# Kernel tuning notes

Measured on AMD Instinct MI355X. Metric: run time of the kernel, lower is better.

Reference implementation:

```python
import jax, jax.numpy as jnp
import numpy as np

N = 50000      # nodes
E = 1600000    # edges (avg degree 32)
F = 64         # input node features
H = 128        # GAT hidden dim (heads=1)
A = 16         # action dim
ED = 2         # edge feature dim


def setup_inputs() -> dict:
    key = jax.random.key(0)
    ks = jax.random.split(key, 20)
    def w(k, shape, fan_in):
        return jax.random.normal(k, shape, jnp.float32) * (1.0 / np.sqrt(fan_in))
    return {
        "x": jax.random.normal(ks[0], (N, F), jnp.float32),
        "edge_index": jax.random.randint(ks[1], (2, E), 0, N, dtype=jnp.int32),
        "edge_attr": jax.random.normal(ks[2], (E, ED), jnp.float32),
        # GATConv layer 1 (F -> H)
        "W1": w(ks[3], (F, H), F),
        "We1": w(ks[4], (ED, H), ED),
        "asrc1": w(ks[5], (H,), H),
        "adst1": w(ks[6], (H,), H),
        "aedge1": w(ks[7], (H,), H),
        "b1": jnp.zeros((H,), jnp.float32),
        # GATConv layer 2 (H -> H)
        "W2": w(ks[8], (H, H), H),
        "We2": w(ks[9], (ED, H), ED),
        "asrc2": w(ks[10], (H,), H),
        "adst2": w(ks[11], (H,), H),
        "aedge2": w(ks[12], (H,), H),
        "b2": jnp.zeros((H,), jnp.float32),
        # final head
        "Wfc": w(ks[13], (H, A), H),
        "bfc": jnp.zeros((A,), jnp.float32),
    }


def _gat_layer(x, src, dst, ea, W, We, a_s, a_d, a_e, b, n):
    """PyG GATConv, heads=1: gather -> attn logits -> segment softmax -> scatter-add."""
    h = x @ W                      # [n, H]
    he = ea @ We                   # [E', H]
    logits = jax.nn.leaky_relu(
        (h * a_s).sum(-1)[src] + (h * a_d).sum(-1)[dst] + (he * a_e).sum(-1),
        negative_slope=0.2,
    )                              # [E']
    m = jax.ops.segment_max(logits, dst, num_segments=n)
    p = jnp.exp(logits - m[dst])
    denom = jax.ops.segment_sum(p, dst, num_segments=n)
    alpha = p / (denom[dst] + 1e-16)
    out = jax.ops.segment_sum(h[src] * alpha[:, None], dst, num_segments=n)
    return out + b


def reference(x, edge_index, edge_attr, W1, We1, asrc1, adst1, aedge1, b1,
              W2, We2, asrc2, adst2, aedge2, b2, Wfc, bfc):
    n = x.shape[0]
    src0, dst0 = edge_index[0], edge_index[1]
    # add_self_loops=True with fill_value='mean': self-loop edge_attr is the
    # mean of incoming edge_attr per destination node (0 if no incoming edges)
    cnt = jax.ops.segment_sum(jnp.ones_like(dst0, dtype=edge_attr.dtype), dst0, num_segments=n)
    ea_mean = jax.ops.segment_sum(edge_attr, dst0, num_segments=n) / jnp.maximum(cnt, 1.0)[:, None]
    loops = jnp.arange(n, dtype=src0.dtype)
    src = jnp.concatenate([src0, loops])
    dst = jnp.concatenate([dst0, loops])
    ea = jnp.concatenate([edge_attr, ea_mean], axis=0)

    h = jax.nn.relu(_gat_layer(x, src, dst, ea, W1, We1, asrc1, adst1, aedge1, b1, n))
    h = jax.nn.relu(_gat_layer(h, src, dst, ea, W2, We2, asrc2, adst2, aedge2, b2, n))
    pooled = h.mean(axis=0)        # [H]
    return jnp.tanh(pooled @ Wfc + bfc)
```

## Files before the change

### kernel.cpp

```cpp
#include <hip/hip_runtime.h>
#include <math.h>

#define H_DIM 128
#define BWID 128
#define BMAX 512
#define CHUNK 4096

typedef int v4i __attribute__((ext_vector_type(4)));

__global__ void prep_kernel(const float* __restrict__ We1, const float* __restrict__ ae1,
                            const float* __restrict__ We2, const float* __restrict__ ae2,
                            const float* __restrict__ W1, const float* __restrict__ as1,
                            const float* __restrict__ ad1,
                            const float* __restrict__ W2, const float* __restrict__ as2,
                            const float* __restrict__ ad2,
                            float* __restrict__ c, float* __restrict__ vs1,
                            float* __restrict__ vd1, float* __restrict__ vs2,
                            float* __restrict__ vd2) {
    int t = threadIdx.x;
    if (t < 64) {
        float s = 0.f, d = 0.f;
        for (int h = 0; h < 128; ++h) {
            float w = W1[t * 128 + h];
            s += w * as1[h];
            d += w * ad1[h];
        }
        vs1[t] = s; vd1[t] = d;
    } else if (t < 192) {
        int k = t - 64;
        float s = 0.f, d = 0.f;
        for (int h = 0; h < 128; ++h) {
            float w = W2[k * 128 + h];
            s += w * as2[h];
            d += w * ad2[h];
        }
        vs2[k] = s; vd2[k] = d;
    } else {
        int l = t - 192;
        float a1x = ae1[l], a1y = ae1[l + 64];
        float a2x = ae2[l], a2y = ae2[l + 64];
        float v0 = We1[l] * a1x + We1[l + 64] * a1y;
        float v1 = We1[128 + l] * a1x + We1[192 + l] * a1y;
        float v2 = We2[l] * a2x + We2[l + 64] * a2y;
        float v3 = We2[128 + l] * a2x + We2[192 + l] * a2y;
        for (int off = 32; off; off >>= 1) {
            v0 += __shfl_xor(v0, off);
            v1 += __shfl_xor(v1, off);
            v2 += __shfl_xor(v2, off);
            v3 += __shfl_xor(v3, off);
        }
        if (l == 0) { c[0] = v0; c[1] = v1; c[2] = v2; c[3] = v3; }
    }
}

__global__ __launch_bounds__(256) void count_kernel(const int* __restrict__ ei,
                                                    int* __restrict__ gcnt, int E, int B) {
    __shared__ int hist[BMAX];
    int tid = threadIdx.x;
    for (int i = tid; i < B; i += 256) hist[i] = 0;
    __syncthreads();
    int lo = blockIdx.x * CHUNK, hi = min(lo + CHUNK, E);
    for (int e = lo + tid; e < hi; e += 256)
        atomicAdd(&hist[ei[E + e] >> 7], 1);
    __syncthreads();
    for (int i = tid; i < B; i += 256)
        if (hist[i]) atomicAdd(&gcnt[i], hist[i]);
}

__global__ void bscan_kernel(const int* __restrict__ gcnt, int* __restrict__ bstart,
                             int* __restrict__ gcur, int* __restrict__ rowptr,
                             int B, int n, int E) {
    __shared__ int s[BMAX];
    int t = threadIdx.x;
    int v0 = (t < B) ? gcnt[t] : 0;
    s[t] = v0;
    __syncthreads();
    for (int off = 1; off < BMAX; off <<= 1) {
        int v = (t >= off) ? s[t - off] : 0;
        __syncthreads();
        s[t] += v;
        __syncthreads();
    }
    if (t < B) {
        int excl = s[t] - v0;
        bstart[t] = excl;
        gcur[t] = excl;
    }
    if (t == 0) { bstart[B] = E; rowptr[n] = E; }
}

__global__ __launch_bounds__(256) void bin_kernel(const int* __restrict__ ei,
                                                  const float* __restrict__ ea,
                                                  const float* __restrict__ cvec,
                                                  int* __restrict__ gcur,
                                                  int4* __restrict__ binned, int E, int B) {
    __shared__ int cnt[BMAX];
    __shared__ int base[BMAX];
    int tid = threadIdx.x;
    for (int i = tid; i < B; i += 256) cnt[i] = 0;
    __syncthreads();
    int lo = blockIdx.x * CHUNK, hi = min(lo + CHUNK, E);
    for (int e = lo + tid; e < hi; e += 256)
        atomicAdd(&cnt[ei[E + e] >> 7], 1);
    __syncthreads();
    for (int i = tid; i < B; i += 256) {
        int c = cnt[i];
        base[i] = c ? atomicAdd(&gcur[i], c) : 0;
        cnt[i] = 0;
    }
    __syncthreads();
    float c0 = cvec[0], c1 = cvec[1], c2 = cvec[2], c3 = cvec[3];
    for (int e = lo + tid; e < hi; e += 256) {
        int s = ei[e], d = ei[E + e];
        float2 v = ((const float2*)ea)[e];
        float d1 = c0 * v.x + c1 * v.y;
        float d2 = c2 * v.x + c3 * v.y;
        int b = d >> 7;
        int loc = atomicAdd(&cnt[b], 1);
        binned[(size_t)(base[b] + loc)] = make_int4(s, d, __float_as_int(d1), __float_as_int(d2));
    }
}

__global__ __launch_bounds__(256) void build_kernel(const int* __restrict__ bstart,
                                                    const int4* __restrict__ binned,
                                                    int* __restrict__ rowptr,
                                                    int4* __restrict__ csr, int n) {
    __shared__ int cnt[BWID];
    __shared__ int sc[BWID];
    __shared__ int cur[BWID];
    int b = blockIdx.x, tid = threadIdx.x;
    int d0 = b << 7;
    int lo = bstart[b], hi = bstart[b + 1];
    if (tid < BWID) cnt[tid] = 0;
    __syncthreads();
    for (int k = lo + tid; k < hi; k += 256)
        atomicAdd(&cnt[binned[k].y & (BWID - 1)], 1);
    __syncthreads();
    if (tid < BWID) sc[tid] = cnt[tid];
    __syncthreads();
    for (int off = 1; off < BWID; off <<= 1) {
        int v = (tid < BWID && tid >= off) ? sc[tid - off] : 0;
        __syncthreads();
        if (tid < BWID) sc[tid] += v;
        __syncthreads();
    }
    if (tid < BWID) {
        int excl = sc[tid] - cnt[tid];
        cur[tid] = lo + excl;
        int d = d0 + tid;
        if (d < n) rowptr[d] = lo + excl;
    }
    __syncthreads();
    for (int k = lo + tid; k < hi; k += 256) {
        int4 e = binned[k];
        int slot = atomicAdd(&cur[e.y & (BWID - 1)], 1);
        csr[slot] = make_int4(e.x, e.z, e.w, 0);
    }
}

__global__ void hshd64_kernel(const float* __restrict__ x, const float* __restrict__ vs,
                              const float* __restrict__ vd, float* __restrict__ hs,
                              float* __restrict__ hd, int n) {
    int w = (blockIdx.x * blockDim.x + threadIdx.x) >> 6;
    int lane = threadIdx.x & 63;
    if (w >= n) return;
    float xv = x[(size_t)w * 64 + lane];
    float ss = xv * vs[lane];
    float sd = xv * vd[lane];
    for (int off = 32; off; off >>= 1) {
        ss += __shfl_xor(ss, off);
        sd += __shfl_xor(sd, off);
    }
    if (lane == 0) { hs[w] = ss; hd[w] = sd; }
}

__global__ __launch_bounds__(256) void agg64_kernel(
        const int* __restrict__ rowptr, const int4* __restrict__ csr,
        const float* __restrict__ hs, const float* __restrict__ hd,
        const float* __restrict__ feat, float* __restrict__ t_out, int n) {
    int w = (blockIdx.x * blockDim.x + threadIdx.x) >> 6;
    int lane = threadIdx.x & 63;
    if (w >= n) return;
    int beg = rowptr[w], end = rowptr[w + 1];
    int len = end - beg;
    float hdv = hd[w], hsw = hs[w];
    int g = lane >> 4;
    int c16 = lane & 15;
    float4 acc = make_float4(0.f, 0.f, 0.f, 0.f);
    float m, scale, lself;

    if (len <= 64) {
        bool valid = lane < len;
        int4 c4 = valid ? csr[beg + lane] : make_int4(0, 0, 0, 0);
        float ed = valid ? __int_as_float(c4.y) : 0.f;
        float l = hs[c4.x] + hdv + ed;
        l = (l >= 0.f) ? l : 0.2f * l;
        float mymax = valid ? l : -1e30f;
        float edsum = ed;
        for (int off = 32; off; off >>= 1) {
            mymax = fmaxf(mymax, __shfl_xor(mymax, off));
            edsum += __shfl_xor(edsum, off);
        }
        lself = hsw + hdv + edsum / fmaxf((float)len, 1.0f);
        lself = (lself >= 0.f) ? lself : 0.2f * lself;
        m = fmaxf(mymax, lself);
        float p = valid ? __expf(l - m) : 0.f;
        float psum = p;
        for (int off = 32; off; off >>= 1) psum += __shfl_xor(psum, off);
        psum += __expf(lself - m);
        scale = 1.f / (psum + 1e-16f);
        float pn = p * scale;
        int src = c4.x;
        for (int j = g; j < len; j += 4) {
            float a = __shfl(pn, j);
            int sj = __shfl(src, j);
            const float4 hv = *(const float4*)&feat[(size_t)sj * 64 + c16 * 4];
            acc.x += a * hv.x; acc.y += a * hv.y; acc.z += a * hv.z; acc.w += a * hv.w;
        }
    } else {
        float mymax = -1e30f, edsum = 0.f;
        for (int base = beg; base < end; base += 64) {
            int k = base + lane;
            if (k < end) {
                int4 c4 = csr[k];
                float ed = __int_as_float(c4.y);
                edsum += ed;
                float l = hs[c4.x] + hdv + ed;
                l = (l >= 0.f) ? l : 0.2f * l;
                mymax = fmaxf(mymax, l);
            }
        }
        for (int off = 32; off; off >>= 1) {
            mymax = fmaxf(mymax, __shfl_xor(mymax, off));
            edsum += __shfl_xor(edsum, off);
        }
        lself = hsw + hdv + edsum / fmaxf((float)len, 1.0f);
        lself = (lself >= 0.f) ? lself : 0.2f * lself;
        m = fmaxf(mymax, lself);
        float psum = 0.f;
        for (int base = beg; base < end; base += 64) {
            int k = base + lane;
            if (k < end) {
                int4 c4 = csr[k];
                float l = hs[c4.x] + hdv + __int_as_float(c4.y);
                l = (l >= 0.f) ? l : 0.2f * l;
                psum += __expf(l - m);
            }
        }
        for (int off = 32; off; off >>= 1) psum += __shfl_xor(psum, off);
        psum += __expf(lself - m);
        scale = 1.f / (psum + 1e-16f);
        for (int base = beg; base < end; base += 64) {
            int k = base + lane;
            float pn = 0.f; int src = 0;
            if (k < end) {
                int4 c4 = csr[k];
                float l = hs[c4.x] + hdv + __int_as_float(c4.y);
                l = (l >= 0.f) ? l : 0.2f * l;
                pn = __expf(l - m) * scale;
                src = c4.x;
            }
            int cl = min(end - base, 64);
            for (int j = g; j < cl; j += 4) {
                float a = __shfl(pn, j);
                int sj = __shfl(src, j);
                const float4 hv = *(const float4*)&feat[(size_t)sj * 64 + c16 * 4];
                acc.x += a * hv.x; acc.y += a * hv.y; acc.z += a * hv.z; acc.w += a * hv.w;
            }
        }
    }
    if (g == 0) {
        float a = __expf(lself - m) * scale;
        const float4 hv = *(const float4*)&feat[(size_t)w * 64 + c16 * 4];
        acc.x += a * hv.x; acc.y += a * hv.y; acc.z += a * hv.z; acc.w += a * hv.w;
    }
    float4 p1, p2, p3;
    p1.x = __shfl(acc.x, c16 + 16); p1.y = __shfl(acc.y, c16 + 16);
    p1.z = __shfl(acc.z, c16 + 16); p1.w = __shfl(acc.w, c16 + 16);
    p2.x = __shfl(acc.x, c16 + 32); p2.y = __shfl(acc.y, c16 + 32);
    p2.z = __shfl(acc.z, c16 + 32); p2.w = __shfl(acc.w, c16 + 32);
    p3.x = __shfl(acc.x, c16 + 48); p3.y = __shfl(acc.y, c16 + 48);
    p3.z = __shfl(acc.z, c16 + 48); p3.w = __shfl(acc.w, c16 + 48);
    if (lane < 16) {
        float4 o;
        o.x = acc.x + p1.x + p2.x + p3.x;
        o.y = acc.y + p1.y + p2.y + p3.y;
        o.z = acc.z + p1.z + p2.z + p3.z;
        o.w = acc.w + p1.w + p2.w + p3.w;
        *(float4*)&t_out[(size_t)w * 64 + c16 * 4] = o;
    }
}

__global__ __launch_bounds__(256) void agg128_kernel(
        const int* __restrict__ rowptr, const int4* __restrict__ csr,
        const float* __restrict__ hs, const float* __restrict__ hd,
        const float* __restrict__ feat, float* __restrict__ t_out, int n) {
    int w = (blockIdx.x * blockDim.x + threadIdx.x) >> 6;
    int lane = threadIdx.x & 63;
    if (w >= n) return;
    int beg = rowptr[w], end = rowptr[w + 1];
    int len = end - beg;
    float hdv = hd[w], hsw = hs[w];
    int half = lane >> 5;
    int col = lane & 31;
    float4 acc = make_float4(0.f, 0.f, 0.f, 0.f);
    float m, scale, lself;

    if (len <= 64) {
        bool valid = lane < len;
        int4 c4 = valid ? csr[beg + lane] : make_int4(0, 0, 0, 0);
        float ed = valid ? __int_as_float(c4.z) : 0.f;
        float l = hs[c4.x] + hdv + ed;
        l = (l >= 0.f) ? l : 0.2f * l;
        float mymax = valid ? l : -1e30f;
        float edsum = ed;
        for (int off = 32; off; off >>= 1) {
            mymax = fmaxf(mymax, __shfl_xor(mymax, off));
            edsum += __shfl_xor(edsum, off);
        }
        lself = hsw + hdv + edsum / fmaxf((float)len, 1.0f);
        lself = (lself >= 0.f) ? lself : 0.2f * lself;
        m = fmaxf(mymax, lself);
        float p = valid ? __expf(l - m) : 0.f;
        float psum = p;
        for (int off = 32; off; off >>= 1) psum += __shfl_xor(psum, off);
        psum += __expf(lself - m);
        scale = 1.f / (psum + 1e-16f);
        float pn = p * scale;
        int src = c4.x;
        for (int j = half; j < len; j += 2) {
            float a = __shfl(pn, j);
            int sj = __shfl(src, j);
            const float4 hv = *(const float4*)&feat[(size_t)sj * H_DIM + col * 4];
            acc.x += a * hv.x; acc.y += a * hv.y; acc.z += a * hv.z; acc.w += a * hv.w;
        }
    } else {
        float mymax = -1e30f, edsum = 0.f;
        for (int base = beg; base < end; base += 64) {
            int k = base + lane;
            if (k < end) {
                int4 c4 = csr[k];
                float ed = __int_as_float(c4.z);
                edsum += ed;
                float l = hs[c4.x] + hdv + ed;
                l = (l >= 0.f) ? l : 0.2f * l;
                mymax = fmaxf(mymax, l);
            }
        }
        for (int off = 32; off; off >>= 1) {
            mymax = fmaxf(mymax, __shfl_xor(mymax, off));
            edsum += __shfl_xor(edsum, off);
        }
        lself = hsw + hdv + edsum / fmaxf((float)len, 1.0f);
        lself = (lself >= 0.f) ? lself : 0.2f * lself;
        m = fmaxf(mymax, lself);
        float psum = 0.f;
        for (int base = beg; base < end; base += 64) {
            int k = base + lane;
            if (k < end) {
                int4 c4 = csr[k];
                float l = hs[c4.x] + hdv + __int_as_float(c4.z);
                l = (l >= 0.f) ? l : 0.2f * l;
                psum += __expf(l - m);
            }
        }
        for (int off = 32; off; off >>= 1) psum += __shfl_xor(psum, off);
        psum += __expf(lself - m);
        scale = 1.f / (psum + 1e-16f);
        for (int base = beg; base < end; base += 64) {
            int k = base + lane;
            float pn = 0.f; int src = 0;
            if (k < end) {
                int4 c4 = csr[k];
                float l = hs[c4.x] + hdv + __int_as_float(c4.z);
                l = (l >= 0.f) ? l : 0.2f * l;
                pn = __expf(l - m) * scale;
                src = c4.x;
            }
            int cl = min(end - base, 64);
            for (int j = half; j < cl; j += 2) {
                float a = __shfl(pn, j);
                int sj = __shfl(src, j);
                const float4 hv = *(const float4*)&feat[(size_t)sj * H_DIM + col * 4];
                acc.x += a * hv.x; acc.y += a * hv.y; acc.z += a * hv.z; acc.w += a * hv.w;
            }
        }
    }
    if (half == 0) {
        float a = __expf(lself - m) * scale;
        const float4 hv = *(const float4*)&feat[(size_t)w * H_DIM + col * 4];
        acc.x += a * hv.x; acc.y += a * hv.y; acc.z += a * hv.z; acc.w += a * hv.w;
    }
    float4 oth;
    oth.x = __shfl(acc.x, col + 32);
    oth.y = __shfl(acc.y, col + 32);
    oth.z = __shfl(acc.z, col + 32);
    oth.w = __shfl(acc.w, col + 32);
    if (half == 0) {
        float4 o;
        o.x = acc.x + oth.x; o.y = acc.y + oth.y;
        o.z = acc.z + oth.z; o.w = acc.w + oth.w;
        *(float4*)&t_out[(size_t)w * H_DIM + col * 4] = o;
    }
}

template <int FIN, bool DO_HSHD>
__global__ __launch_bounds__(256) void gemm_kernel(const float* __restrict__ X,
                                                   const float* __restrict__ W,
                                                   const float* __restrict__ bias,
                                                   const float* __restrict__ vs,
                                                   const float* __restrict__ vd,
                                                   float* __restrict__ Hout,
                                                   float* __restrict__ hs,
                                                   float* __restrict__ hd, int n) {
    __shared__ float xs[32 * FIN];
    int tid = threadIdx.x;
    int r0 = blockIdx.x * 32;
    for (int idx = tid; idx < 32 * FIN; idx += 256) {
        int r = idx / FIN, k = idx - r * FIN;
        int row = r0 + r;
        xs[idx] = (row < n) ? X[(size_t)row * FIN + k] : 0.0f;
    }
    __syncthreads();
    int tcol = tid & 31;
    int trow = tid >> 5;
    float acc[4][4] = {{0.f}};
    const float* wp = W + tcol * 4;
    const float* x0p = &xs[(trow * 4 + 0) * FIN];
    const float* x1p = &xs[(trow * 4 + 1) * FIN];
    const float* x2p = &xs[(trow * 4 + 2) * FIN];
    const float* x3p = &xs[(trow * 4 + 3) * FIN];
#pragma unroll 8
    for (int k = 0; k < FIN; ++k) {
        float4 w4 = *(const float4*)(wp + k * H_DIM);
        float x0 = x0p[k], x1 = x1p[k], x2 = x2p[k], x3 = x3p[k];
        acc[0][0] += x0 * w4.x; acc[0][1] += x0 * w4.y; acc[0][2] += x0 * w4.z; acc[0][3] += x0 * w4.w;
        acc[1][0] += x1 * w4.x; acc[1][1] += x1 * w4.y; acc[1][2] += x1 * w4.z; acc[1][3] += x1 * w4.w;
        acc[2][0] += x2 * w4.x; acc[2][1] += x2 * w4.y; acc[2][2] += x2 * w4.z; acc[2][3] += x2 * w4.w;
        acc[3][0] += x3 * w4.x; acc[3][1] += x3 * w4.y; acc[3][2] += x3 * w4.z; acc[3][3] += x3 * w4.w;
    }
    float4 b4 = *(const float4*)&bias[tcol * 4];
    float4 vs4, vd4;
    if (DO_HSHD) {
        vs4 = *(const float4*)&vs[tcol * 4];
        vd4 = *(const float4*)&vd[tcol * 4];
    }
#pragma unroll
    for (int r = 0; r < 4; ++r) {
        int row = r0 + trow * 4 + r;
        float4 o;
        o.x = fmaxf(acc[r][0] + b4.x, 0.f);
        o.y = fmaxf(acc[r][1] + b4.y, 0.f);
        o.z = fmaxf(acc[r][2] + b4.z, 0.f);
        o.w = fmaxf(acc[r][3] + b4.w, 0.f);
        if (row < n) *(float4*)&Hout[(size_t)row * H_DIM + tcol * 4] = o;
        if (DO_HSHD) {
            float ss = o.x * vs4.x + o.y * vs4.y + o.z * vs4.z + o.w * vs4.w;
            float sd = o.x * vd4.x + o.y * vd4.y + o.z * vd4.z + o.w * vd4.w;
            for (int off = 16; off; off >>= 1) {
                ss += __shfl_xor(ss, off);
                sd += __shfl_xor(sd, off);
            }
            if (tcol == 0 && row < n) { hs[row] = ss; hd[row] = sd; }
        }
    }
}

__global__ void pool_kernel(const float* __restrict__ hmat, float* __restrict__ pooled,
                            int n) {
    __shared__ float red[256];
    int col = threadIdx.x & 127;
    int half = threadIdx.x >> 7;
    int rows_per_block = (n + gridDim.x - 1) / gridDim.x;
    int r0 = blockIdx.x * rows_per_block;
    int r1 = min(r0 + rows_per_block, n);
    float s = 0.f;
    for (int r = r0 + half; r < r1; r += 2) s += hmat[(size_t)r * H_DIM + col];
    red[threadIdx.x] = s;
    __syncthreads();
    if (half == 0) atomicAdd(&pooled[col], red[threadIdx.x] + red[threadIdx.x + 128]);
}

__global__ void final_kernel(const float* __restrict__ pooled, const float* __restrict__ Wfc,
                             const float* __restrict__ bfc, float* __restrict__ out, int n) {
    int t = threadIdx.x;
    if (t >= 16) return;
    float inv_n = 1.0f / (float)n;
    float s = 0.f;
    for (int j = 0; j < 128; ++j) s += pooled[j] * inv_n * Wfc[j * 16 + t];
    out[t] = tanhf(s + bfc[t]);
}

extern "C" void kernel_launch(void* const* d_in, const int* in_sizes, int n_in,
                              void* d_out, int out_size, void* d_ws, size_t ws_size,
                              hipStream_t stream) {
    const float* x   = (const float*)d_in[0];
    const int*   ei  = (const int*)d_in[1];
    const float* ea  = (const float*)d_in[2];
    const float* W1  = (const float*)d_in[3];
    const float* We1 = (const float*)d_in[4];
    const float* as1 = (const float*)d_in[5];
    const float* ad1 = (const float*)d_in[6];
    const float* ae1 = (const float*)d_in[7];
    const float* b1  = (const float*)d_in[8];
    const float* W2  = (const float*)d_in[9];
    const float* We2 = (const float*)d_in[10];
    const float* as2 = (const float*)d_in[11];
    const float* ad2 = (const float*)d_in[12];
    const float* ae2 = (const float*)d_in[13];
    const float* b2  = (const float*)d_in[14];
    const float* Wfc = (const float*)d_in[15];
    const float* bfc = (const float*)d_in[16];
    float* out = (float*)d_out;

    const int n = in_sizes[0] / 64;
    const int E = in_sizes[1] / 2;
    const int B = (n + BWID - 1) / BWID;

    size_t o = 0;
    auto alloc = [&](size_t count) { size_t r = o; o += (count + 63) & ~(size_t)63; return r; };
    size_t o_gcnt   = alloc(BMAX);
    size_t o_bstart = alloc(BMAX + 1);
    size_t o_gcur   = alloc(BMAX);
    size_t o_rowptr = alloc(n + 1);
    size_t o_csr    = alloc(4 * (size_t)E);
    size_t o_hs     = alloc(n);
    size_t o_hd     = alloc(n);
    size_t o_bufA   = alloc((size_t)n * H_DIM);
    size_t o_bufB   = alloc((size_t)n * H_DIM);
    size_t o_c      = alloc(4);
    size_t o_vs1    = alloc(64);
    size_t o_vd1    = alloc(64);
    size_t o_vs2    = alloc(128);
    size_t o_vd2    = alloc(128);
    size_t o_pool   = alloc(128);
    (void)ws_size;
    int4* binned = (int4*)((float*)d_ws + o_bufA);

    float* wsf = (float*)d_ws;
    hipMemsetAsync(wsf + o_gcnt, 0, BMAX * sizeof(int), stream);
    hipMemsetAsync(wsf + o_pool, 0, 128 * sizeof(float), stream);

    prep_kernel<<<1, 256, 0, stream>>>(We1, ae1, We2, ae2, W1, as1, ad1, W2, as2, ad2,
        wsf + o_c, wsf + o_vs1, wsf + o_vd1, wsf + o_vs2, wsf + o_vd2);

    int ebg = (E + CHUNK - 1) / CHUNK;
    count_kernel<<<ebg, 256, 0, stream>>>(ei, (int*)(wsf + o_gcnt), E, B);
    bscan_kernel<<<1, BMAX, 0, stream>>>((int*)(wsf + o_gcnt), (int*)(wsf + o_bstart),
        (int*)(wsf + o_gcur), (int*)(wsf + o_rowptr), B, n, E);
    bin_kernel<<<ebg, 256, 0, stream>>>(ei, ea, wsf + o_c, (int*)(wsf + o_gcur),
        binned, E, B);
    build_kernel<<<B, 256, 0, stream>>>((int*)(wsf + o_bstart), binned,
        (int*)(wsf + o_rowptr), (int4*)(wsf + o_csr), n);

    int wgrid = (n + 3) / 4;

    hshd64_kernel<<<wgrid, 256, 0, stream>>>(x, wsf + o_vs1, wsf + o_vd1,
        wsf + o_hs, wsf + o_hd, n);
    agg64_kernel<<<wgrid, 256, 0, stream>>>((int*)(wsf + o_rowptr), (const int4*)(wsf + o_csr),
        wsf + o_hs, wsf + o_hd, x, wsf + o_bufB, n);
    gemm_kernel<64, true><<<(n + 31) / 32, 256, 0, stream>>>(wsf + o_bufB, W1, b1,
        wsf + o_vs2, wsf + o_vd2, wsf + o_bufA, wsf + o_hs, wsf + o_hd, n);

    agg128_kernel<<<wgrid, 256, 0, stream>>>((int*)(wsf + o_rowptr), (const int4*)(wsf + o_csr),
        wsf + o_hs, wsf + o_hd, wsf + o_bufA, wsf + o_bufB, n);
    gemm_kernel<128, false><<<(n + 31) / 32, 256, 0, stream>>>(wsf + o_bufB, W2, b2,
        nullptr, nullptr, wsf + o_bufA, nullptr, nullptr, n);

    pool_kernel<<<256, 256, 0, stream>>>(wsf + o_bufA, wsf + o_pool, n);
    final_kernel<<<1, 64, 0, stream>>>(wsf + o_pool, Wfc, bfc, out, n);
}
```

Baseline: 454.4 us.

## Store node features and edge records in fp16 to halve gather traffic

Node features gathered during aggregation (input x, layer-1 output, aggregated intermediates) are now stored as fp16 and converted to fp32 on load. The binned and CSR edge records shrink from int4 to int2 by packing the source index with the local destination in the binning pass and storing the two edge logit terms as a half2. The aim is to cut memory bandwidth in the gather-heavy aggregation kernels and in CSR construction. The cost is reduced precision and an extra conversion pass over x. Packing the source into 16 bits truncates indices at or above 65536, which holds for N=50000 but not for larger graphs.

```diff
diff --git a/kernel.cpp b/kernel.cpp
--- a/kernel.cpp
+++ b/kernel.cpp
@@ -1,12 +1,11 @@
 #include <hip/hip_runtime.h>
+#include <hip/hip_fp16.h>
 #include <math.h>
 
 #define H_DIM 128
 #define BWID 128
 #define BMAX 512
 #define CHUNK 4096
-
-typedef int v4i __attribute__((ext_vector_type(4)));
 
 __global__ void prep_kernel(const float* __restrict__ We1, const float* __restrict__ ae1,
                             const float* __restrict__ We2, const float* __restrict__ ae2,
@@ -93,7 +92,7 @@
                                                   const float* __restrict__ ea,
                                                   const float* __restrict__ cvec,
                                                   int* __restrict__ gcur,
-                                                  int4* __restrict__ binned, int E, int B) {
+                                                  int2* __restrict__ binned, int E, int B) {
     __shared__ int cnt[BMAX];
     __shared__ int base[BMAX];
     int tid = threadIdx.x;
@@ -115,16 +114,17 @@
         float2 v = ((const float2*)ea)[e];
         float d1 = c0 * v.x + c1 * v.y;
         float d2 = c2 * v.x + c3 * v.y;
+        __half2 hh = __floats2half2_rn(d1, d2);
         int b = d >> 7;
         int loc = atomicAdd(&cnt[b], 1);
-        binned[(size_t)(base[b] + loc)] = make_int4(s, d, __float_as_int(d1), __float_as_int(d2));
+        binned[(size_t)(base[b] + loc)] = make_int2(s | ((d & 127) << 16), *(int*)&hh);
     }
 }
 
 __global__ __launch_bounds__(256) void build_kernel(const int* __restrict__ bstart,
-                                                    const int4* __restrict__ binned,
+                                                    const int2* __restrict__ binned,
                                                     int* __restrict__ rowptr,
-                                                    int4* __restrict__ csr, int n) {
+                                                    int2* __restrict__ csr, int n) {
     __shared__ int cnt[BWID];
     __shared__ int sc[BWID];
     __shared__ int cur[BWID];
@@ -134,7 +134,7 @@
     if (tid < BWID) cnt[tid] = 0;
     __syncthreads();
     for (int k = lo + tid; k < hi; k += 256)
-        atomicAdd(&cnt[binned[k].y & (BWID - 1)], 1);
+        atomicAdd(&cnt[(binned[k].x >> 16) & (BWID - 1)], 1);
     __syncthreads();
     if (tid < BWID) sc[tid] = cnt[tid];
     __syncthreads();
@@ -152,19 +152,20 @@
     }
     __syncthreads();
     for (int k = lo + tid; k < hi; k += 256) {
-        int4 e = binned[k];
-        int slot = atomicAdd(&cur[e.y & (BWID - 1)], 1);
-        csr[slot] = make_int4(e.x, e.z, e.w, 0);
+        int2 e = binned[k];
+        int slot = atomicAdd(&cur[(e.x >> 16) & (BWID - 1)], 1);
+        csr[slot] = make_int2(e.x & 0xFFFF, e.y);
     }
 }
 
 __global__ void hshd64_kernel(const float* __restrict__ x, const float* __restrict__ vs,
                               const float* __restrict__ vd, float* __restrict__ hs,
-                              float* __restrict__ hd, int n) {
+                              float* __restrict__ hd, __half* __restrict__ xh, int n) {
     int w = (blockIdx.x * blockDim.x + threadIdx.x) >> 6;
     int lane = threadIdx.x & 63;
     if (w >= n) return;
     float xv = x[(size_t)w * 64 + lane];
+    xh[(size_t)w * 64 + lane] = __float2half(xv);
     float ss = xv * vs[lane];
     float sd = xv * vd[lane];
     for (int off = 32; off; off >>= 1) {
@@ -175,9 +176,9 @@
 }
 
 __global__ __launch_bounds__(256) void agg64_kernel(
-        const int* __restrict__ rowptr, const int4* __restrict__ csr,
+        const int* __restrict__ rowptr, const int2* __restrict__ csr,
         const float* __restrict__ hs, const float* __restrict__ hd,
-        const float* __restrict__ feat, float* __restrict__ t_out, int n) {
+        const __half* __restrict__ feat, __half* __restrict__ t_out, int n) {
     int w = (blockIdx.x * blockDim.x + threadIdx.x) >> 6;
     int lane = threadIdx.x & 63;
     if (w >= n) return;
@@ -191,9 +192,10 @@
 
     if (len <= 64) {
         bool valid = lane < len;
-        int4 c4 = valid ? csr[beg + lane] : make_int4(0, 0, 0, 0);
-        float ed = valid ? __int_as_float(c4.y) : 0.f;
-        float l = hs[c4.x] + hdv + ed;
+        int2 c2 = valid ? csr[beg + lane] : make_int2(0, 0);
+        __half2 dd = *(__half2*)&c2.y;
+        float ed = valid ? __half2float(dd.x) : 0.f;
+        float l = hs[c2.x] + hdv + ed;
         l = (l >= 0.f) ? l : 0.2f * l;
         float mymax = valid ? l : -1e30f;
         float edsum = ed;
@@ -210,22 +212,28 @@
         psum += __expf(lself - m);
         scale = 1.f / (psum + 1e-16f);
         float pn = p * scale;
-        int src = c4.x;
+        int src = c2.x;
         for (int j = g; j < len; j += 4) {
             float a = __shfl(pn, j);
             int sj = __shfl(src, j);
-            const float4 hv = *(const float4*)&feat[(size_t)sj * 64 + c16 * 4];
-            acc.x += a * hv.x; acc.y += a * hv.y; acc.z += a * hv.z; acc.w += a * hv.w;
+            float2 raw = *(const float2*)&feat[(size_t)sj * 64 + c16 * 4];
+            __half2 h01 = *(__half2*)&raw.x;
+            __half2 h23 = *(__half2*)&raw.y;
+            float2 f01 = __half22float2(h01);
+            float2 f23 = __half22float2(h23);
+            acc.x += a * f01.x; acc.y += a * f01.y;
+            acc.z += a * f23.x; acc.w += a * f23.y;
         }
     } else {
         float mymax = -1e30f, edsum = 0.f;
         for (int base = beg; base < end; base += 64) {
             int k = base + lane;
             if (k < end) {
-                int4 c4 = csr[k];
-                float ed = __int_as_float(c4.y);
+                int2 c2 = csr[k];
+                __half2 dd = *(__half2*)&c2.y;
+                float ed = __half2float(dd.x);
                 edsum += ed;
-                float l = hs[c4.x] + hdv + ed;
+                float l = hs[c2.x] + hdv + ed;
                 l = (l >= 0.f) ? l : 0.2f * l;
                 mymax = fmaxf(mymax, l);
             }
@@ -241,8 +249,9 @@
         for (int base = beg; base < end; base += 64) {
             int k = base + lane;
             if (k < end) {
-                int4 c4 = csr[k];
-                float l = hs[c4.x] + hdv + __int_as_float(c4.y);
+                int2 c2 = csr[k];
+                __half2 dd = *(__half2*)&c2.y;
+                float l = hs[c2.x] + hdv + __half2float(dd.x);
                 l = (l >= 0.f) ? l : 0.2f * l;
                 psum += __expf(l - m);
             }
@@ -254,25 +263,36 @@
             int k = base + lane;
             float pn = 0.f; int src = 0;
             if (k < end) {
-                int4 c4 = csr[k];
-                float l = hs[c4.x] + hdv + __int_as_float(c4.y);
+                int2 c2 = csr[k];
+                __half2 dd = *(__half2*)&c2.y;
+                float l = hs[c2.x] + hdv + __half2float(dd.x);
                 l = (l >= 0.f) ? l : 0.2f * l;
                 pn = __expf(l - m) * scale;
-                src = c4.x;
+                src = c2.x;
             }
             int cl = min(end - base, 64);
             for (int j = g; j < cl; j += 4) {
                 float a = __shfl(pn, j);
                 int sj = __shfl(src, j);
-                const float4 hv = *(const float4*)&feat[(size_t)sj * 64 + c16 * 4];
-                acc.x += a * hv.x; acc.y += a * hv.y; acc.z += a * hv.z; acc.w += a * hv.w;
+                float2 raw = *(const float2*)&feat[(size_t)sj * 64 + c16 * 4];
+                __half2 h01 = *(__half2*)&raw.x;
+                __half2 h23 = *(__half2*)&raw.y;
+                float2 f01 = __half22float2(h01);
+                float2 f23 = __half22float2(h23);
+                acc.x += a * f01.x; acc.y += a * f01.y;
+                acc.z += a * f23.x; acc.w += a * f23.y;
             }
         }
     }
     if (g == 0) {
         float a = __expf(lself - m) * scale;
-        const float4 hv = *(const float4*)&feat[(size_t)w * 64 + c16 * 4];
-        acc.x += a * hv.x; acc.y += a * hv.y; acc.z += a * hv.z; acc.w += a * hv.w;
+        float2 raw = *(const float2*)&feat[(size_t)w * 64 + c16 * 4];
+        __half2 h01 = *(__half2*)&raw.x;
+        __half2 h23 = *(__half2*)&raw.y;
+        float2 f01 = __half22float2(h01);
+        float2 f23 = __half22float2(h23);
+        acc.x += a * f01.x; acc.y += a * f01.y;
+        acc.z += a * f23.x; acc.w += a * f23.y;
     }
     float4 p1, p2, p3;
     p1.x = __shfl(acc.x, c16 + 16); p1.y = __shfl(acc.y, c16 + 16);
@@ -287,14 +307,17 @@
         o.y = acc.y + p1.y + p2.y + p3.y;
         o.z = acc.z + p1.z + p2.z + p3.z;
         o.w = acc.w + p1.w + p2.w + p3.w;
-        *(float4*)&t_out[(size_t)w * 64 + c16 * 4] = o;
+        __half2 q0 = __floats2half2_rn(o.x, o.y);
+        __half2 q1 = __floats2half2_rn(o.z, o.w);
+        int2 st; st.x = *(int*)&q0; st.y = *(int*)&q1;
+        *(int2*)&t_out[(size_t)w * 64 + c16 * 4] = st;
     }
 }
 
 __global__ __launch_bounds__(256) void agg128_kernel(
-        const int* __restrict__ rowptr, const int4* __restrict__ csr,
+        const int* __restrict__ rowptr, const int2* __restrict__ csr,
         const float* __restrict__ hs, const float* __restrict__ hd,
-        const float* __restrict__ feat, float* __restrict__ t_out, int n) {
+        const __half* __restrict__ feat, __half* __restrict__ t_out, int n) {
     int w = (blockIdx.x * blockDim.x + threadIdx.x) >> 6;
     int lane = threadIdx.x & 63;
     if (w >= n) return;
@@ -308,9 +331,10 @@
 
     if (len <= 64) {
         bool valid = lane < len;
-        int4 c4 = valid ? csr[beg + lane] : make_int4(0, 0, 0, 0);
-        float ed = valid ? __int_as_float(c4.z) : 0.f;
-        float l = hs[c4.x] + hdv + ed;
+        int2 c2 = valid ? csr[beg + lane] : make_int2(0, 0);
+        __half2 dd = *(__half2*)&c2.y;
+        float ed = valid ? __half2float(dd.y) : 0.f;
+        float l = hs[c2.x] + hdv + ed;
         l = (l >= 0.f) ? l : 0.2f * l;
         float mymax = valid ? l : -1e30f;
         float edsum = ed;
@@ -327,22 +351,28 @@
         psum += __expf(lself - m);
         scale = 1.f / (psum + 1e-16f);
         float pn = p * scale;
-        int src = c4.x;
+        int src = c2.x;
         for (int j = half; j < len; j += 2) {
             float a = __shfl(pn, j);
             int sj = __shfl(src, j);
-            const float4 hv = *(const float4*)&feat[(size_t)sj * H_DIM + col * 4];
-            acc.x += a * hv.x; acc.y += a * hv.y; acc.z += a * hv.z; acc.w += a * hv.w;
+            float2 raw = *(const float2*)&feat[(size_t)sj * H_DIM + col * 4];
+            __half2 h01 = *(__half2*)&raw.x;
+            __half2 h23 = *(__half2*)&raw.y;
+            float2 f01 = __half22float2(h01);
+            float2 f23 = __half22float2(h23);
+            acc.x += a * f01.x; acc.y += a * f01.y;
+            acc.z += a * f23.x; acc.w += a * f23.y;
         }
     } else {
         float mymax = -1e30f, edsum = 0.f;
         for (int base = beg; base < end; base += 64) {
             int k = base + lane;
             if (k < end) {
-                int4 c4 = csr[k];
-                float ed = __int_as_float(c4.z);
+                int2 c2 = csr[k];
+                __half2 dd = *(__half2*)&c2.y;
+                float ed = __half2float(dd.y);
                 edsum += ed;
-                float l = hs[c4.x] + hdv + ed;
+                float l = hs[c2.x] + hdv + ed;
                 l = (l >= 0.f) ? l : 0.2f * l;
                 mymax = fmaxf(mymax, l);
             }
@@ -358,8 +388,9 @@
         for (int base = beg; base < end; base += 64) {
             int k = base + lane;
             if (k < end) {
-                int4 c4 = csr[k];
-                float l = hs[c4.x] + hdv + __int_as_float(c4.z);
+                int2 c2 = csr[k];
+                __half2 dd = *(__half2*)&c2.y;
+                float l = hs[c2.x] + hdv + __half2float(dd.y);
                 l = (l >= 0.f) ? l : 0.2f * l;
                 psum += __expf(l - m);
             }
@@ -371,25 +402,36 @@
             int k = base + lane;
             float pn = 0.f; int src = 0;
             if (k < end) {
-                int4 c4 = csr[k];
-                float l = hs[c4.x] + hdv + __int_as_float(c4.z);
+                int2 c2 = csr[k];
+                __half2 dd = *(__half2*)&c2.y;
+                float l = hs[c2.x] + hdv + __half2float(dd.y);
                 l = (l >= 0.f) ? l : 0.2f * l;
                 pn = __expf(l - m) * scale;
-                src = c4.x;
+                src = c2.x;
             }
             int cl = min(end - base, 64);
             for (int j = half; j < cl; j += 2) {
                 float a = __shfl(pn, j);
                 int sj = __shfl(src, j);
-                const float4 hv = *(const float4*)&feat[(size_t)sj * H_DIM + col * 4];
-                acc.x += a * hv.x; acc.y += a * hv.y; acc.z += a * hv.z; acc.w += a * hv.w;
+                float2 raw = *(const float2*)&feat[(size_t)sj * H_DIM + col * 4];
+                __half2 h01 = *(__half2*)&raw.x;
+                __half2 h23 = *(__half2*)&raw.y;
+                float2 f01 = __half22float2(h01);
+                float2 f23 = __half22float2(h23);
+                acc.x += a * f01.x; acc.y += a * f01.y;
+                acc.z += a * f23.x; acc.w += a * f23.y;
             }
         }
     }
     if (half == 0) {
         float a = __expf(lself - m) * scale;
-        const float4 hv = *(const float4*)&feat[(size_t)w * H_DIM + col * 4];
-        acc.x += a * hv.x; acc.y += a * hv.y; acc.z += a * hv.z; acc.w += a * hv.w;
+        float2 raw = *(const float2*)&feat[(size_t)w * H_DIM + col * 4];
+        __half2 h01 = *(__half2*)&raw.x;
+        __half2 h23 = *(__half2*)&raw.y;
+        float2 f01 = __half22float2(h01);
+        float2 f23 = __half22float2(h23);
+        acc.x += a * f01.x; acc.y += a * f01.y;
+        acc.z += a * f23.x; acc.w += a * f23.y;
     }
     float4 oth;
     oth.x = __shfl(acc.x, col + 32);
@@ -400,26 +442,44 @@
         float4 o;
         o.x = acc.x + oth.x; o.y = acc.y + oth.y;
         o.z = acc.z + oth.z; o.w = acc.w + oth.w;
-        *(float4*)&t_out[(size_t)w * H_DIM + col * 4] = o;
-    }
-}
-
-template <int FIN, bool DO_HSHD>
-__global__ __launch_bounds__(256) void gemm_kernel(const float* __restrict__ X,
+        __half2 q0 = __floats2half2_rn(o.x, o.y);
+        __half2 q1 = __floats2half2_rn(o.z, o.w);
+        int2 st; st.x = *(int*)&q0; st.y = *(int*)&q1;
+        *(int2*)&t_out[(size_t)w * H_DIM + col * 4] = st;
+    }
+}
+
+template <int FIN, bool DO_HSHD, bool OUT_HALF>
+__global__ __launch_bounds__(256) void gemm_kernel(const __half* __restrict__ X,
                                                    const float* __restrict__ W,
                                                    const float* __restrict__ bias,
                                                    const float* __restrict__ vs,
                                                    const float* __restrict__ vd,
-                                                   float* __restrict__ Hout,
+                                                   void* __restrict__ HoutV,
                                                    float* __restrict__ hs,
                                                    float* __restrict__ hd, int n) {
     __shared__ float xs[32 * FIN];
     int tid = threadIdx.x;
     int r0 = blockIdx.x * 32;
-    for (int idx = tid; idx < 32 * FIN; idx += 256) {
-        int r = idx / FIN, k = idx - r * FIN;
+    constexpr int NV = 32 * FIN / 8;
+    for (int idx = tid; idx < NV; idx += 256) {
+        int r = (idx * 8) / FIN, k = idx * 8 - r * FIN;
         int row = r0 + r;
-        xs[idx] = (row < n) ? X[(size_t)row * FIN + k] : 0.0f;
+        float* p = &xs[r * FIN + k];
+        if (row < n) {
+            int4 raw = *(const int4*)&X[(size_t)row * FIN + k];
+            __half2 h0 = *(__half2*)&raw.x;
+            __half2 h1 = *(__half2*)&raw.y;
+            __half2 h2 = *(__half2*)&raw.z;
+            __half2 h3 = *(__half2*)&raw.w;
+            float2 f0 = __half22float2(h0), f1 = __half22float2(h1);
+            float2 f2 = __half22float2(h2), f3 = __half22float2(h3);
+            p[0] = f0.x; p[1] = f0.y; p[2] = f1.x; p[3] = f1.y;
+            p[4] = f2.x; p[5] = f2.y; p[6] = f3.x; p[7] = f3.y;
+        } else {
+#pragma unroll
+            for (int q = 0; q < 8; ++q) p[q] = 0.f;
+        }
     }
     __syncthreads();
     int tcol = tid & 31;
@@ -453,7 +513,16 @@
         o.y = fmaxf(acc[r][1] + b4.y, 0.f);
         o.z = fmaxf(acc[r][2] + b4.z, 0.f);
         o.w = fmaxf(acc[r][3] + b4.w, 0.f);
-        if (row < n) *(float4*)&Hout[(size_t)row * H_DIM + tcol * 4] = o;
+        if (row < n) {
+            if (OUT_HALF) {
+                __half2 q0 = __floats2half2_rn(o.x, o.y);
+                __half2 q1 = __floats2half2_rn(o.z, o.w);
+                int2 st; st.x = *(int*)&q0; st.y = *(int*)&q1;
+                *(int2*)((__half*)HoutV + (size_t)row * H_DIM + tcol * 4) = st;
+            } else {
+                *(float4*)((float*)HoutV + (size_t)row * H_DIM + tcol * 4) = o;
+            }
+        }
         if (DO_HSHD) {
             float ss = o.x * vs4.x + o.y * vs4.y + o.z * vs4.z + o.w * vs4.w;
             float sd = o.x * vd4.x + o.y * vd4.y + o.z * vd4.z + o.w * vd4.w;
@@ -523,11 +592,14 @@
     size_t o_bstart = alloc(BMAX + 1);
     size_t o_gcur   = alloc(BMAX);
     size_t o_rowptr = alloc(n + 1);
-    size_t o_csr    = alloc(4 * (size_t)E);
+    size_t o_csr    = alloc(2 * (size_t)E);
+    size_t o_bufA   = alloc((size_t)n * H_DIM);
+    size_t o_xh     = alloc((size_t)n * 32);
+    size_t o_t1h    = alloc((size_t)n * 32);
+    size_t o_o1h    = alloc((size_t)n * 64);
+    size_t o_t2h    = alloc((size_t)n * 64);
     size_t o_hs     = alloc(n);
     size_t o_hd     = alloc(n);
-    size_t o_bufA   = alloc((size_t)n * H_DIM);
-    size_t o_bufB   = alloc((size_t)n * H_DIM);
     size_t o_c      = alloc(4);
     size_t o_vs1    = alloc(64);
     size_t o_vd1    = alloc(64);
@@ -535,9 +607,10 @@
     size_t o_vd2    = alloc(128);
     size_t o_pool   = alloc(128);
     (void)ws_size;
-    int4* binned = (int4*)((float*)d_ws + o_bufA);
-
     float* wsf = (float*)d_ws;
+    int2* binned = (int2*)(wsf + o_bufA);
+    int2* csr2   = (int2*)(wsf + o_csr);
+
     hipMemsetAsync(wsf + o_gcnt, 0, BMAX * sizeof(int), stream);
     hipMemsetAsync(wsf + o_pool, 0, 128 * sizeof(float), stream);
 
@@ -551,21 +624,23 @@
     bin_kernel<<<ebg, 256, 0, stream>>>(ei, ea, wsf + o_c, (int*)(wsf + o_gcur),
         binned, E, B);
     build_kernel<<<B, 256, 0, stream>>>((int*)(wsf + o_bstart), binned,
-        (int*)(wsf + o_rowptr), (int4*)(wsf + o_csr), n);
+        (int*)(wsf + o_rowptr), csr2, n);
 
     int wgrid = (n + 3) / 4;
 
     hshd64_kernel<<<wgrid, 256, 0, stream>>>(x, wsf + o_vs1, wsf + o_vd1,
-        wsf + o_hs, wsf + o_hd, n);
-    agg64_kernel<<<wgrid, 256, 0, stream>>>((int*)(wsf + o_rowptr), (const int4*)(wsf + o_csr),
-        wsf + o_hs, wsf + o_hd, x, wsf + o_bufB, n);
-    gemm_kernel<64, true><<<(n + 31) / 32, 256, 0, stream>>>(wsf + o_bufB, W1, b1,
-        wsf + o_vs2, wsf + o_vd2, wsf + o_bufA, wsf + o_hs, wsf + o_hd, n);
-
-    agg128_kernel<<<wgrid, 256, 0, stream>>>((int*)(wsf + o_rowptr), (const int4*)(wsf + o_csr),
-        wsf + o_hs, wsf + o_hd, wsf + o_bufA, wsf + o_bufB, n);
-    gemm_kernel<128, false><<<(n + 31) / 32, 256, 0, stream>>>(wsf + o_bufB, W2, b2,
-        nullptr, nullptr, wsf + o_bufA, nullptr, nullptr, n);
+        wsf + o_hs, wsf + o_hd, (__half*)(wsf + o_xh), n);
+    agg64_kernel<<<wgrid, 256, 0, stream>>>((int*)(wsf + o_rowptr), csr2,
+        wsf + o_hs, wsf + o_hd, (const __half*)(wsf + o_xh), (__half*)(wsf + o_t1h), n);
+    gemm_kernel<64, true, true><<<(n + 31) / 32, 256, 0, stream>>>(
+        (const __half*)(wsf + o_t1h), W1, b1, wsf + o_vs2, wsf + o_vd2,
+        (void*)(wsf + o_o1h), wsf + o_hs, wsf + o_hd, n);
+
+    agg128_kernel<<<wgrid, 256, 0, stream>>>((int*)(wsf + o_rowptr), csr2,
+        wsf + o_hs, wsf + o_hd, (const __half*)(wsf + o_o1h), (__half*)(wsf + o_t2h), n);
+    gemm_kernel<128, false, false><<<(n + 31) / 32, 256, 0, stream>>>(
+        (const __half*)(wsf + o_t2h), W2, b2, nullptr, nullptr,
+        (void*)(wsf + o_bufA), nullptr, nullptr, n);
 
     pool_kernel<<<256, 256, 0, stream>>>(wsf + o_bufA, wsf + o_pool, n);
     final_kernel<<<1, 64, 0, stream>>>(wsf + o_pool, Wfc, bfc, out, n);
```

After: 377.7 us. 16.9% less time.
